# Optimization experiments

Hardware: AMD Instinct MI355X
Metric: run time of the kernel (lower is better)

## Reference

```python
import jax, jax.numpy as jnp
import numpy as np

B, L, F, H = 1024, 256, 128, 256
A, CH, OUT = 128, 256, 512


def setup_inputs() -> dict:
    key = jax.random.key(0)
    ks = jax.random.split(key, 12)
    s = lambda k, shape, fan: (jax.random.normal(k, shape, jnp.float32) / np.float32(np.sqrt(fan)))
    return dict(
        input_batch=jax.random.normal(ks[0], (B, L, F), jnp.float32),
        tte=jax.random.randint(ks[1], (B,), 0, L, jnp.int32),
        W_ih=s(ks[2], (3 * H, F), F), W_hh=s(ks[3], (3 * H, H), H),
        b_ih=jnp.zeros((3 * H,), jnp.float32), b_hh=jnp.zeros((3 * H,), jnp.float32),
        W_out=s(ks[4], (F, H), H), b_out=jnp.zeros((F,), jnp.float32),
        Wa=s(ks[5], (H, A), H), Ua=s(ks[6], (F, A), F), va=s(ks[7], (A,), A),
        W1=s(ks[8], (H + F, CH), H + F), b1=jnp.zeros((CH,), jnp.float32),
        W2=s(ks[9], (CH, OUT), CH), b2=jnp.zeros((OUT,), jnp.float32),
    )


def _gru_step(x, h, W_ih, W_hh, b_ih, b_hh):
    # torch.nn.GRU single-step math, batched over B
    gi = x @ W_ih.T + b_ih          # [B,3H]
    gh = h @ W_hh.T + b_hh          # [B,3H]
    i_r, i_z, i_n = jnp.split(gi, 3, axis=-1)
    h_r, h_z, h_n = jnp.split(gh, 3, axis=-1)
    r = jax.nn.sigmoid(i_r + h_r)
    z = jax.nn.sigmoid(i_z + h_z)
    n = jnp.tanh(i_n + r * h_n)
    return (1.0 - z) * n + z * h


def reference(input_batch, tte, W_ih, W_hh, b_ih, b_hh, W_out, b_out,
              Wa, Ua, va, W1, b1, W2, b2):
    Bn, Ln, Fn = input_batch.shape
    Hn = W_hh.shape[1]
    h0 = jnp.zeros((Bn, Hn), input_batch.dtype)
    xs = jnp.moveaxis(input_batch, 1, 0)  # [L,B,F]
    ts = jnp.arange(Ln)

    def step(h, inp):
        x_t, t = inp
        h_new = _gru_step(x_t, h, W_ih, W_hh, b_ih, b_hh)
        active = (t < tte)[:, None]          # ragged length mask [B,1]
        h = jnp.where(active, h_new, h)      # freeze state past tte
        out_t = jnp.where(active, h_new @ W_out.T + b_out, 0.0)
        hid_t = jnp.where(active, h_new, 0.0)
        return h, (out_t, hid_t)

    _, (outs, hids) = jax.lax.scan(step, h0, (xs, ts))
    output_batch = jnp.moveaxis(outs, 0, 1)   # [B,L,F], zero-padded like the torch code
    hidden_vec = jnp.moveaxis(hids, 0, 1)     # [B,L,H], zero-padded

    # last measurement at index tte (the torch code indexes batch[tte])
    last = jnp.take_along_axis(input_batch, tte[:, None, None].astype(jnp.int32), axis=1)[:, 0]  # [B,F]

    # decoder: additive attention over the full padded trajectory
    scores = jnp.tanh(hidden_vec @ Wa + (last @ Ua)[:, None, :]) @ va   # [B,L]
    alpha = jax.nn.softmax(scores, axis=-1)
    context = jnp.einsum('bl,blh->bh', alpha, hidden_vec)               # [B,H]

    # causes network: MLP + softmax over cause x time-bin grid
    zc = jax.nn.relu(jnp.concatenate([context, last], axis=-1) @ W1 + b1)
    fht = jax.nn.softmax(zc @ W2 + b2, axis=-1)                         # [B,OUT]
    return output_batch, fht
```

## Files before the change

kernel.cpp:

```cpp
#include <hip/hip_runtime.h>

#define B_ 1024
#define L_ 256
#define F_ 128
#define H_ 256

typedef __bf16 bf16x8 __attribute__((ext_vector_type(8)));
typedef __bf16 bf16x4 __attribute__((ext_vector_type(4)));
typedef float f32x4 __attribute__((ext_vector_type(4)));
typedef int i32x4 __attribute__((ext_vector_type(4)));

#define MFMA16(a, b, c) __builtin_amdgcn_mfma_f32_16x16x32_bf16((a), (b), (c), 0, 0, 0)
#define MFMA_I8(a, b, c) __builtin_amdgcn_mfma_i32_16x16x64_i8((a), (b), (c), 0, 0, 0)
#define BAR_LDS() asm volatile("s_waitcnt lgkmcnt(0)\n\ts_barrier" ::: "memory")

__device__ __forceinline__ float rcp_f(float x) { return __builtin_amdgcn_rcpf(x); }
__device__ __forceinline__ float sigm(float x) { return rcp_f(1.f + __expf(-x)); }
__device__ __forceinline__ float tanh_f(float x) {
  float ax = fabsf(x);
  float e = __expf(-2.f * ax);
  float r = (1.f - e) * rcp_f(1.f + e);
  return copysignf(r, x);
}
__device__ __forceinline__ bf16x8 ld8(const __bf16* p) { return *(const bf16x8*)p; }
__device__ __forceinline__ float wave_max(float v) {
#pragma unroll
  for (int d = 1; d < 64; d <<= 1) v = fmaxf(v, __shfl_xor(v, d));
  return v;
}
__device__ __forceinline__ float wave_sum(float v) {
#pragma unroll
  for (int d = 1; d < 64; d <<= 1) v += __shfl_xor(v, d);
  return v;
}
__device__ __forceinline__ unsigned pack4(float a, float b, float c, float d, float inv) {
  return (unsigned)(unsigned char)(signed char)__float2int_rn(a * inv)
       | ((unsigned)(unsigned char)(signed char)__float2int_rn(b * inv) << 8)
       | ((unsigned)(unsigned char)(signed char)__float2int_rn(c * inv) << 16)
       | ((unsigned)(unsigned char)(signed char)__float2int_rn(d * inv) << 24);
}
__device__ __forceinline__ void wait_flag(int* flags, int idx) {
  int guard = 0;
  while (__hip_atomic_load(&flags[idx], __ATOMIC_ACQUIRE, __HIP_MEMORY_SCOPE_AGENT) == 0)
    if (++guard > 2000000) break;
}

__global__ void cvt_kernel(const float* __restrict__ wih_f, const float* __restrict__ wout_f,
                           const float* __restrict__ wa_f, const float* __restrict__ ua_f,
                           const float* __restrict__ w1_f, const float* __restrict__ w2_f,
                           __bf16* __restrict__ wih, __bf16* __restrict__ wout,
                           __bf16* __restrict__ wa_t, __bf16* __restrict__ ua_t,
                           __bf16* __restrict__ w1_t, __bf16* __restrict__ w2_t) {
  int i = blockIdx.x * 256 + threadIdx.x;
  if (i < 98304) wih[i] = (__bf16)wih_f[i];
  else if (i < 131072) wout[i - 98304] = (__bf16)wout_f[i - 98304];
  else if (i < 163840) {
    int j = i - 131072; int a = j >> 8, k = j & 255;
    wa_t[j] = (__bf16)wa_f[k * 128 + a];
  } else if (i < 180224) {
    int j = i - 163840; int a = j >> 7, f = j & 127;
    ua_t[j] = (__bf16)ua_f[f * 128 + a];
  } else if (i < 278528) {
    int j = i - 180224; int c = j / 384, k = j - c * 384;
    w1_t[j] = (__bf16)w1_f[k * 256 + c];
  } else if (i < 409600) {
    int j = i - 278528; int o = j >> 8, k = j & 255;
    w2_t[j] = (__bf16)w2_f[k * 512 + o];
  }
}

__global__ void quant_kernel(const float* __restrict__ whh_f,
                             signed char* __restrict__ wq_rz,
                             signed char* __restrict__ wqn_f,
                             float* __restrict__ dq) {
  const int c = blockIdx.x * 256 + threadIdx.x;
  if (c >= 768) return;
  const float* row = whh_f + (size_t)c * 256;
  float m = 0.f;
  for (int k4 = 0; k4 < 64; ++k4) {
    float4 v = *(const float4*)(row + k4 * 4);
    m = fmaxf(m, fmaxf(fmaxf(fabsf(v.x), fabsf(v.y)), fmaxf(fabsf(v.z), fabsf(v.w))));
  }
  const float inv = (m > 1e-30f) ? 127.f / m : 0.f;
  dq[c] = m / 16129.f;
  if (c < 512) {
    for (int k4 = 0; k4 < 64; ++k4) {
      float4 v = *(const float4*)(row + k4 * 4);
      *(unsigned*)(wq_rz + (size_t)c * 256 + k4 * 4) = pack4(v.x, v.y, v.z, v.w, inv);
    }
  } else {
    const int cN = c - 512;
    const int base0 = (cN >> 4) * 4, l15q = cN & 15;
    for (int kt = 0; kt < 4; ++kt)
      for (int lgq = 0; lgq < 4; ++lgq) {
        signed char* dst = wqn_f + (size_t)(((base0 + kt) * 64) + lgq * 16 + l15q) * 16;
        const float* src = row + kt * 64 + lgq * 16;
        for (int j4 = 0; j4 < 4; ++j4) {
          float4 v = *(const float4*)(src + j4 * 4);
          *(unsigned*)(dst + j4 * 4) = pack4(v.x, v.y, v.z, v.w, inv);
        }
      }
  }
}

__global__ __launch_bounds__(1024) void mega_kernel(
    const float* __restrict__ x, const int* __restrict__ tte,
    const float* __restrict__ b_ih, const float* __restrict__ b_hh,
    const __bf16* __restrict__ wih,
    const signed char* __restrict__ wq_rz, const signed char* __restrict__ wqn_f,
    const float* __restrict__ dq, __bf16* __restrict__ gi,
    const __bf16* __restrict__ wout, const float* __restrict__ b_out,
    __bf16* __restrict__ hid, float* __restrict__ out, int* __restrict__ flags) {
  __shared__ signed char wlds[512 * 256];
  __shared__ signed char hb[2][16][272];
  __shared__ __bf16 hbf[2][16][260];
  const int tid = threadIdx.x;

  if (blockIdx.x >= 64) {
    const int pid = blockIdx.x - 64;
    const int bblk = pid & 63, tgrp = pid >> 6;
    const int b0 = bblk * 16;
    int tmaxB = 0;
    for (int i = 0; i < 16; ++i) tmaxB = max(tmaxB, tte[b0 + i]);
    if (tid < 512 && tgrp * 16 <= tmaxB) {
      const int lane = tid & 63, w = tid >> 6;
      const int l15 = lane & 15, lg = lane >> 4, kofs = lg * 8;
      bf16x8 wf[6][4];
      float bias[6];
#pragma unroll
      for (int tile = 0; tile < 6; ++tile) {
        const int gate = tile >> 1;
        const int c = w * 32 + (tile & 1) * 16 + l15;
        const int col = gate * 256 + c;
#pragma unroll
        for (int kt = 0; kt < 4; ++kt)
          wf[tile][kt] = ld8(wih + (size_t)col * 128 + kt * 32 + kofs);
        bias[tile] = (gate == 0) ? b_ih[c] + b_hh[c]
                   : (gate == 1) ? b_ih[256 + c] + b_hh[256 + c]
                                 : b_ih[512 + c];
      }
#pragma unroll 1
      for (int ti = 0; ti < 16; ++ti) {
        const int t = tgrp * 16 + ti;
        if (t > tmaxB) break;
        const float* xb = x + ((size_t)(b0 + l15) * L_ + t) * F_ + kofs;
        bf16x8 xfr[4];
#pragma unroll
        for (int kt = 0; kt < 4; ++kt) {
          float4 a = *(const float4*)(xb + kt * 32);
          float4 b = *(const float4*)(xb + kt * 32 + 4);
          xfr[kt][0] = (__bf16)a.x; xfr[kt][1] = (__bf16)a.y;
          xfr[kt][2] = (__bf16)a.z; xfr[kt][3] = (__bf16)a.w;
          xfr[kt][4] = (__bf16)b.x; xfr[kt][5] = (__bf16)b.y;
          xfr[kt][6] = (__bf16)b.z; xfr[kt][7] = (__bf16)b.w;
        }
        f32x4 acc[6];
#pragma unroll
        for (int tile = 0; tile < 6; ++tile) {
          acc[tile][0] = bias[tile]; acc[tile][1] = bias[tile];
          acc[tile][2] = bias[tile]; acc[tile][3] = bias[tile];
        }
#pragma unroll
        for (int kt = 0; kt < 4; ++kt)
#pragma unroll
          for (int tile = 0; tile < 6; ++tile)
            acc[tile] = MFMA16(xfr[kt], wf[tile][kt], acc[tile]);
        const size_t chunk = (((size_t)t * 64 + bblk) * 8 + w) * 6;
#pragma unroll
        for (int tile = 0; tile < 6; ++tile) {
          bf16x4 pk;
          pk[0] = (__bf16)acc[tile][0]; pk[1] = (__bf16)acc[tile][1];
          pk[2] = (__bf16)acc[tile][2]; pk[3] = (__bf16)acc[tile][3];
          *(bf16x4*)(gi + (chunk + tile) * 256 + (lg * 16 + l15) * 4) = pk;
        }
      }
    }
    __syncthreads();
    if (tid == 0)
      __hip_atomic_store(&flags[pid], 1, __ATOMIC_RELEASE, __HIP_MEMORY_SCOPE_AGENT);
    return;
  }

  const int lane = tid & 63, w = tid >> 6;
  const int l15 = lane & 15, lg = lane >> 4, kofs = lg * 8;
  const int b0 = blockIdx.x * 16;

  for (int idx = tid; idx < 8192; idx += 1024) {
    const int row = idx >> 4, g = idx & 15;
    uint4 v = *(const uint4*)(wq_rz + (size_t)row * 256 + g * 16);
    *(uint4*)&wlds[row * 256 + ((g ^ (row & 15)) << 4)] = v;
  }
  for (int i = tid; i < 2 * 16 * 272; i += 1024) ((signed char*)hb)[i] = 0;

  const int colL = w * 16 + l15;
  const float dqR = dq[colL], dqZ = dq[256 + colL], dqN = dq[512 + colL];
  const float bhn = b_hh[512 + colL];

  int tteC[4];
#pragma unroll
  for (int r = 0; r < 4; ++r) tteC[r] = tte[b0 + 4 * lg + r];
  const int rowS = (tid >> 5) & 15, segS = tid & 31;
  const int tteS = tte[b0 + rowS];
  int tmax = 0;
  for (int i = 0; i < 16; ++i) tmax = max(tmax, tte[b0 + i]);

  i32x4 nw[4];
#pragma unroll
  for (int kt = 0; kt < 4; ++kt)
    nw[kt] = *(const i32x4*)(wqn_f + (size_t)((w * 4 + kt) * 64 + lane) * 16);

  const int ocol = (w & 7) * 16 + l15;
  bf16x8 wof[8];
#pragma unroll
  for (int kt = 0; kt < 8; ++kt)
    wof[kt] = ld8(wout + (size_t)ocol * 256 + kt * 32 + kofs);
  const float bo = b_out[ocol];

  __bf16* hidp = hid + ((size_t)(b0 + rowS) * L_) * H_ + segS * 8;
  float* outp = out + ((size_t)(b0 + 4 * lg) * L_) * F_ + ocol;

  float hprev[4] = {0.f, 0.f, 0.f, 0.f};

  if (tid == 0) wait_flag(flags, blockIdx.x);
  __syncthreads();

  const __bf16* gib = gi + (((size_t)blockIdx.x * 8 + (w >> 1)) * 6 + (w & 1)) * 256
                    + (lg * 16 + l15) * 4;
  bf16x4 g0 = *(const bf16x4*)(gib);
  bf16x4 g1 = *(const bf16x4*)(gib + 512);
  bf16x4 g2 = *(const bf16x4*)(gib + 1024);
  const __bf16* gpp = gib + 786432;

#pragma unroll 1
  for (int t = 0; t < tmax; ++t) {
    const int c = t & 1, nc = c ^ 1;

    if (((t + 1) & 15) == 0) {
      if (tid == 0) wait_flag(flags, (((t + 1) >> 4) << 6) | blockIdx.x);
      __syncthreads();
    }

    const bf16x4 gr = g0, gz = g1, gn = g2;
    g0 = *(const bf16x4*)(gpp);
    g1 = *(const bf16x4*)(gpp + 512);
    g2 = *(const bf16x4*)(gpp + 1024);
    gpp += 786432;

    i32x4 aR = {0, 0, 0, 0}, aZ = {0, 0, 0, 0}, aN = {0, 0, 0, 0};
#pragma unroll
    for (int kt = 0; kt < 4; ++kt) {
      const i32x4 hA = *(const i32x4*)&hb[c][l15][kt * 64 + lg * 16];
      const int gsw = ((kt * 4 + lg) ^ l15) << 4;
      aR = MFMA_I8(hA, *(const i32x4*)&wlds[colL * 256 + gsw], aR);
      aZ = MFMA_I8(hA, *(const i32x4*)&wlds[(256 + colL) * 256 + gsw], aZ);
      aN = MFMA_I8(hA, nw[kt], aN);
    }

#pragma unroll
    for (int r = 0; r < 4; ++r) {
      const int row = 4 * lg + r;
      const float rg = sigm((float)gr[r] + (float)aR[r] * dqR);
      const float zg = sigm((float)gz[r] + (float)aZ[r] * dqZ);
      const float ng = tanh_f((float)gn[r] + rg * ((float)aN[r] * dqN + bhn));
      const float hold = hprev[r];
      const float hnew = zg * (hold - ng) + ng;
      const float hw = (t < tteC[r]) ? hnew : hold;
      hprev[r] = hw;
      hb[nc][row][colL] = (signed char)__float2int_rn(hw * 127.f);
      hbf[nc][row][colL] = (__bf16)hw;
    }
    BAR_LDS();

    if (w < 8) {
      f32x4 acc = {0, 0, 0, 0};
#pragma unroll
      for (int kt = 0; kt < 8; ++kt) {
        const bf16x8 af = *(const bf16x8*)&hbf[nc][l15][kt * 32 + kofs];
        acc = MFMA16(af, wof[kt], acc);
      }
#pragma unroll
      for (int r = 0; r < 4; ++r)
        if (t < tteC[r]) outp[(size_t)r * (L_ * F_)] = acc[r] + bo;
      outp += F_;
    } else {
      if (t < tteS) *(uint4*)hidp = *(const uint4*)&hbf[nc][rowS][segS * 8];
      hidp += H_;
    }
  }
}

__global__ __launch_bounds__(512, 2) void decoder3_kernel(
    const float* __restrict__ x, const int* __restrict__ tte,
    const __bf16* __restrict__ hid, const __bf16* __restrict__ wa_t,
    const __bf16* __restrict__ ua_t, const __bf16* __restrict__ w1_t,
    const __bf16* __restrict__ w2_t, const float* __restrict__ va,
    const float* __restrict__ b1, const float* __restrict__ b2,
    float* __restrict__ fht) {
  __shared__ __bf16 catb[16][392];
  __shared__ float u_s[4][128];
  __shared__ float sa[4][256];
  __shared__ __bf16 z1b[16][264];
  __shared__ float lg2[4][516];
  __shared__ float ctxp[2][4][256];
  __shared__ float va_s[128];
  __shared__ int tte_s[4];
  const int tid = threadIdx.x;
  const int lane = tid & 63, w = tid >> 6;
  const int l15 = lane & 15, lg = lane >> 4, kofs = lg * 8;
  const int b0 = blockIdx.x * 4;

  if (tid < 4) tte_s[tid] = tte[b0 + tid];
  if (tid < 128) va_s[tid] = va[tid];
  if (tid < 392)
    for (int r = 4; r < 16; ++r) catb[r][tid] = (__bf16)0.f;
  if (tid < 264)
    for (int r = 4; r < 16; ++r) z1b[r][tid] = (__bf16)0.f;
  __syncthreads();

  {
    const int row = tid >> 7, c = tid & 127;
    catb[row][256 + c] = (__bf16)x[((size_t)(b0 + row) * L_ + tte_s[row]) * F_ + c];
  }
  __syncthreads();

  {
    f32x4 uacc = {0, 0, 0, 0};
#pragma unroll
    for (int kt = 0; kt < 4; ++kt) {
      const bf16x8 af = *(const bf16x8*)&catb[l15][256 + kt * 32 + kofs];
      const bf16x8 bf = ld8(ua_t + (size_t)(w * 16 + l15) * 128 + kt * 32 + kofs);
      uacc = MFMA16(af, bf, uacc);
    }
#pragma unroll
    for (int r = 0; r < 4; ++r) {
      const int row = 4 * lg + r;
      if (row < 4) u_s[row][w * 16 + l15] = uacc[r];
    }
  }
  __syncthreads();

  bf16x8 zero8;
#pragma unroll
  for (int j = 0; j < 8; ++j) zero8[j] = (__bf16)0.f;
#pragma unroll 1
  for (int it = 0; it < 8; ++it) {
    const int pair = it * 8 + w;
    const int b = pair >> 4, mtile = pair & 15;
    const int tteB = tte_s[b];
    const int trow = mtile * 16 + l15;
    const __bf16* hrow = hid + ((size_t)(b0 + b) * L_ + trow) * H_ + kofs;
    bf16x8 af[8];
#pragma unroll
    for (int kt = 0; kt < 8; ++kt) af[kt] = (trow < tteB) ? ld8(hrow + kt * 32) : zero8;
    f32x4 sacc[8];
#pragma unroll
    for (int ct = 0; ct < 8; ++ct) { sacc[ct][0] = 0; sacc[ct][1] = 0; sacc[ct][2] = 0; sacc[ct][3] = 0; }
#pragma unroll
    for (int kt = 0; kt < 8; ++kt)
#pragma unroll
      for (int ct = 0; ct < 8; ++ct)
        sacc[ct] = MFMA16(af[kt], ld8(wa_t + (size_t)(ct * 16 + l15) * 256 + kt * 32 + kofs), sacc[ct]);
    float sp[4] = {0, 0, 0, 0};
#pragma unroll
    for (int ct = 0; ct < 8; ++ct) {
      const int a = ct * 16 + l15;
      const float ua = u_s[b][a], vv = va_s[a];
#pragma unroll
      for (int r = 0; r < 4; ++r) sp[r] += tanh_f(sacc[ct][r] + ua) * vv;
    }
#pragma unroll
    for (int r = 0; r < 4; ++r) {
      sp[r] += __shfl_xor(sp[r], 1);
      sp[r] += __shfl_xor(sp[r], 2);
      sp[r] += __shfl_xor(sp[r], 4);
      sp[r] += __shfl_xor(sp[r], 8);
    }
    if (l15 == 0) {
#pragma unroll
      for (int r = 0; r < 4; ++r) sa[b][mtile * 16 + 4 * lg + r] = sp[r];
    }
  }
  __syncthreads();

  if (w < 4) {
    float sv[4];
#pragma unroll
    for (int j = 0; j < 4; ++j) sv[j] = sa[w][lane + 64 * j];
    float mx = fmaxf(fmaxf(sv[0], sv[1]), fmaxf(sv[2], sv[3]));
    mx = wave_max(mx);
    float es[4], ss = 0.f;
#pragma unroll
    for (int j = 0; j < 4; ++j) { es[j] = __expf(sv[j] - mx); ss += es[j]; }
    ss = wave_sum(ss);
    const float inv = rcp_f(ss);
#pragma unroll
    for (int j = 0; j < 4; ++j) sa[w][lane + 64 * j] = es[j] * inv;
  }
  __syncthreads();

  {
    const int be = w & 3, half = w >> 2;
    const int tteE = tte_s[be];
    float c4[4] = {0.f, 0.f, 0.f, 0.f};
    const __bf16* hp = hid + ((size_t)(b0 + be) * L_ + half) * H_ + lane * 4;
#pragma unroll 2
    for (int t = half; t < tteE; t += 2) {
      const float al = sa[be][t];
      const bf16x4 hv = *(const bf16x4*)hp;
      hp += 2 * H_;
#pragma unroll
      for (int j = 0; j < 4; ++j) c4[j] += al * (float)hv[j];
    }
#pragma unroll
    for (int j = 0; j < 4; ++j) ctxp[half][be][lane * 4 + j] = c4[j];
  }
  __syncthreads();
  if (w < 4) {
#pragma unroll
    for (int j = 0; j < 4; ++j)
      catb[w][lane * 4 + j] = (__bf16)(ctxp[0][w][lane * 4 + j] + ctxp[1][w][lane * 4 + j]);
  }
  __syncthreads();

#pragma unroll 1
  for (int half = 0; half < 2; ++half) {
    const int nt = w * 2 + half;
    f32x4 zacc = {0, 0, 0, 0};
#pragma unroll
    for (int kt = 0; kt < 12; ++kt) {
      const bf16x8 af = *(const bf16x8*)&catb[l15][kt * 32 + kofs];
      const bf16x8 bf = ld8(w1_t + (size_t)(nt * 16 + l15) * 384 + kt * 32 + kofs);
      zacc = MFMA16(af, bf, zacc);
    }
    const float bb = b1[nt * 16 + l15];
#pragma unroll
    for (int r = 0; r < 4; ++r) {
      const int row = 4 * lg + r;
      if (row < 4) z1b[row][nt * 16 + l15] = (__bf16)fmaxf(zacc[r] + bb, 0.f);
    }
  }
  __syncthreads();

#pragma unroll 1
  for (int q = 0; q < 4; ++q) {
    const int nt = w * 4 + q;
    f32x4 oacc = {0, 0, 0, 0};
#pragma unroll
    for (int kt = 0; kt < 8; ++kt) {
      const bf16x8 af = *(const bf16x8*)&z1b[l15][kt * 32 + kofs];
      const bf16x8 bf = ld8(w2_t + (size_t)(nt * 16 + l15) * 256 + kt * 32 + kofs);
      oacc = MFMA16(af, bf, oacc);
    }
    const float bb = b2[nt * 16 + l15];
#pragma unroll
    for (int r = 0; r < 4; ++r) {
      const int row = 4 * lg + r;
      if (row < 4) lg2[row][nt * 16 + l15] = oacc[r] + bb;
    }
  }
  __syncthreads();
  if (w < 4) {
    float lv[8];
    float mx = -1e30f;
#pragma unroll
    for (int j = 0; j < 8; ++j) { lv[j] = lg2[w][lane + 64 * j]; mx = fmaxf(mx, lv[j]); }
    mx = wave_max(mx);
    float s2 = 0.f;
#pragma unroll
    for (int j = 0; j < 8; ++j) { lv[j] = __expf(lv[j] - mx); s2 += lv[j]; }
    s2 = wave_sum(s2);
    const float inv2 = rcp_f(s2);
#pragma unroll
    for (int j = 0; j < 8; ++j)
      fht[(size_t)(b0 + w) * 512 + lane + 64 * j] = lv[j] * inv2;
  }
}

extern "C" void kernel_launch(void* const* d_in, const int* in_sizes, int n_in,
                              void* d_out, int out_size, void* d_ws, size_t ws_size,
                              hipStream_t stream) {
  const float* x = (const float*)d_in[0];
  const int* tte = (const int*)d_in[1];
  const float* W_ih = (const float*)d_in[2];
  const float* W_hh = (const float*)d_in[3];
  const float* b_ih = (const float*)d_in[4];
  const float* b_hh = (const float*)d_in[5];
  const float* W_out = (const float*)d_in[6];
  const float* b_out = (const float*)d_in[7];
  const float* Wa = (const float*)d_in[8];
  const float* Ua = (const float*)d_in[9];
  const float* va = (const float*)d_in[10];
  const float* W1 = (const float*)d_in[11];
  const float* b1 = (const float*)d_in[12];
  const float* W2 = (const float*)d_in[13];
  const float* b2 = (const float*)d_in[14];

  char* ws = (char*)d_ws;
  __bf16* wih = (__bf16*)(ws + 0);
  __bf16* wout = (__bf16*)(ws + 196608);
  __bf16* wa_t = (__bf16*)(ws + 262144);
  __bf16* ua_t = (__bf16*)(ws + 327680);
  __bf16* w1_t = (__bf16*)(ws + 360448);
  __bf16* w2_t = (__bf16*)(ws + 557056);
  signed char* wq_rz = (signed char*)(ws + 819200);
  signed char* wqn_f = (signed char*)(ws + 950272);
  float* dq = (float*)(ws + 1015808);
  int* flags = (int*)(ws + 1018880);
  __bf16* hid = (__bf16*)(ws + 1048576);
  __bf16* gi = (__bf16*)(ws + 135266304);

  float* out = (float*)d_out;
  float* fht = out + (size_t)33554432;

  hipMemsetAsync(d_out, 0, (size_t)out_size * 4, stream);
  hipMemsetAsync(flags, 0, 4096, stream);
  cvt_kernel<<<1600, 256, 0, stream>>>(W_ih, W_out, Wa, Ua, W1, W2,
                                       wih, wout, wa_t, ua_t, w1_t, w2_t);
  quant_kernel<<<3, 256, 0, stream>>>(W_hh, wq_rz, wqn_f, dq);
  mega_kernel<<<1088, 1024, 0, stream>>>(x, tte, b_ih, b_hh, wih, wq_rz, wqn_f,
                                         dq, gi, wout, b_out, hid, out, flags);
  decoder3_kernel<<<256, 512, 0, stream>>>(x, tte, hid, wa_t, ua_t, w1_t, w2_t,
                                           va, b1, b2, fht);
}
```

Baseline: 876.8 us.

## Split GRU into separate gi GEMM and 4-row recurrent kernel over 256 blocks

Replaces the flag-synchronised megakernel with a standalone input-gate GEMM kernel followed by a recurrent kernel. Each recurrent block now handles 4 batch rows instead of 16, which spreads the sequential recurrence over 256 blocks instead of 64. Gate math is redistributed to one element per thread via an LDS staging buffer, at the cost of an extra barrier per step. The output projection is quantised to int8 MFMA, and the full output memset is replaced by zeroing only the padded rows inside the GEMM kernel. The int8 output projection adds quantisation error, and the GEMM can no longer overlap with the recurrence.

```diff
diff --git a/kernel.cpp b/kernel.cpp
--- a/kernel.cpp
+++ b/kernel.cpp
@@ -39,43 +39,38 @@
        | ((unsigned)(unsigned char)(signed char)__float2int_rn(c * inv) << 16)
        | ((unsigned)(unsigned char)(signed char)__float2int_rn(d * inv) << 24);
 }
-__device__ __forceinline__ void wait_flag(int* flags, int idx) {
-  int guard = 0;
-  while (__hip_atomic_load(&flags[idx], __ATOMIC_ACQUIRE, __HIP_MEMORY_SCOPE_AGENT) == 0)
-    if (++guard > 2000000) break;
-}
-
-__global__ void cvt_kernel(const float* __restrict__ wih_f, const float* __restrict__ wout_f,
-                           const float* __restrict__ wa_f, const float* __restrict__ ua_f,
-                           const float* __restrict__ w1_f, const float* __restrict__ w2_f,
-                           __bf16* __restrict__ wih, __bf16* __restrict__ wout,
-                           __bf16* __restrict__ wa_t, __bf16* __restrict__ ua_t,
-                           __bf16* __restrict__ w1_t, __bf16* __restrict__ w2_t) {
+
+__global__ void cvt_kernel(const float* __restrict__ wih_f, const float* __restrict__ wa_f,
+                           const float* __restrict__ ua_f, const float* __restrict__ w1_f,
+                           const float* __restrict__ w2_f,
+                           __bf16* __restrict__ wih, __bf16* __restrict__ wa_t,
+                           __bf16* __restrict__ ua_t, __bf16* __restrict__ w1_t,
+                           __bf16* __restrict__ w2_t) {
   int i = blockIdx.x * 256 + threadIdx.x;
   if (i < 98304) wih[i] = (__bf16)wih_f[i];
-  else if (i < 131072) wout[i - 98304] = (__bf16)wout_f[i - 98304];
-  else if (i < 163840) {
-    int j = i - 131072; int a = j >> 8, k = j & 255;
+  else if (i < 131072) {
+    int j = i - 98304; int a = j >> 8, k = j & 255;
     wa_t[j] = (__bf16)wa_f[k * 128 + a];
-  } else if (i < 180224) {
-    int j = i - 163840; int a = j >> 7, f = j & 127;
+  } else if (i < 147456) {
+    int j = i - 131072; int a = j >> 7, f = j & 127;
     ua_t[j] = (__bf16)ua_f[f * 128 + a];
-  } else if (i < 278528) {
-    int j = i - 180224; int c = j / 384, k = j - c * 384;
+  } else if (i < 245760) {
+    int j = i - 147456; int c = j / 384, k = j - c * 384;
     w1_t[j] = (__bf16)w1_f[k * 256 + c];
-  } else if (i < 409600) {
-    int j = i - 278528; int o = j >> 8, k = j & 255;
+  } else if (i < 376832) {
+    int j = i - 245760; int o = j >> 8, k = j & 255;
     w2_t[j] = (__bf16)w2_f[k * 512 + o];
   }
 }
 
-__global__ void quant_kernel(const float* __restrict__ whh_f,
+__global__ void quant_kernel(const float* __restrict__ whh_f, const float* __restrict__ wout_f,
                              signed char* __restrict__ wq_rz,
                              signed char* __restrict__ wqn_f,
+                             signed char* __restrict__ wqo_f,
                              float* __restrict__ dq) {
   const int c = blockIdx.x * 256 + threadIdx.x;
-  if (c >= 768) return;
-  const float* row = whh_f + (size_t)c * 256;
+  if (c >= 896) return;
+  const float* row = (c < 768) ? whh_f + (size_t)c * 256 : wout_f + (size_t)(c - 768) * 256;
   float m = 0.f;
   for (int k4 = 0; k4 < 64; ++k4) {
     float4 v = *(const float4*)(row + k4 * 4);
@@ -88,204 +83,223 @@
       float4 v = *(const float4*)(row + k4 * 4);
       *(unsigned*)(wq_rz + (size_t)c * 256 + k4 * 4) = pack4(v.x, v.y, v.z, v.w, inv);
     }
-  } else {
+  } else if (c < 768) {
     const int cN = c - 512;
-    const int base0 = (cN >> 4) * 4, l15q = cN & 15;
+    const int t16 = cN >> 4, l15q = cN & 15;
     for (int kt = 0; kt < 4; ++kt)
       for (int lgq = 0; lgq < 4; ++lgq) {
-        signed char* dst = wqn_f + (size_t)(((base0 + kt) * 64) + lgq * 16 + l15q) * 16;
+        signed char* dst = wqn_f + (size_t)(((t16 * 4 + kt) * 64) + lgq * 16 + l15q) * 16;
         const float* src = row + kt * 64 + lgq * 16;
         for (int j4 = 0; j4 < 4; ++j4) {
           float4 v = *(const float4*)(src + j4 * 4);
           *(unsigned*)(dst + j4 * 4) = pack4(v.x, v.y, v.z, v.w, inv);
         }
       }
-  }
-}
-
-__global__ __launch_bounds__(1024) void mega_kernel(
-    const float* __restrict__ x, const int* __restrict__ tte,
-    const float* __restrict__ b_ih, const float* __restrict__ b_hh,
-    const __bf16* __restrict__ wih,
-    const signed char* __restrict__ wq_rz, const signed char* __restrict__ wqn_f,
-    const float* __restrict__ dq, __bf16* __restrict__ gi,
-    const __bf16* __restrict__ wout, const float* __restrict__ b_out,
-    __bf16* __restrict__ hid, float* __restrict__ out, int* __restrict__ flags) {
-  __shared__ signed char wlds[512 * 256];
-  __shared__ signed char hb[2][16][272];
-  __shared__ __bf16 hbf[2][16][260];
-  const int tid = threadIdx.x;
-
-  if (blockIdx.x >= 64) {
-    const int pid = blockIdx.x - 64;
-    const int bblk = pid & 63, tgrp = pid >> 6;
-    const int b0 = bblk * 16;
-    int tmaxB = 0;
-    for (int i = 0; i < 16; ++i) tmaxB = max(tmaxB, tte[b0 + i]);
-    if (tid < 512 && tgrp * 16 <= tmaxB) {
-      const int lane = tid & 63, w = tid >> 6;
-      const int l15 = lane & 15, lg = lane >> 4, kofs = lg * 8;
-      bf16x8 wf[6][4];
-      float bias[6];
-#pragma unroll
-      for (int tile = 0; tile < 6; ++tile) {
-        const int gate = tile >> 1;
-        const int c = w * 32 + (tile & 1) * 16 + l15;
-        const int col = gate * 256 + c;
-#pragma unroll
-        for (int kt = 0; kt < 4; ++kt)
-          wf[tile][kt] = ld8(wih + (size_t)col * 128 + kt * 32 + kofs);
-        bias[tile] = (gate == 0) ? b_ih[c] + b_hh[c]
-                   : (gate == 1) ? b_ih[256 + c] + b_hh[256 + c]
-                                 : b_ih[512 + c];
-      }
-#pragma unroll 1
-      for (int ti = 0; ti < 16; ++ti) {
-        const int t = tgrp * 16 + ti;
-        if (t > tmaxB) break;
-        const float* xb = x + ((size_t)(b0 + l15) * L_ + t) * F_ + kofs;
-        bf16x8 xfr[4];
-#pragma unroll
-        for (int kt = 0; kt < 4; ++kt) {
-          float4 a = *(const float4*)(xb + kt * 32);
-          float4 b = *(const float4*)(xb + kt * 32 + 4);
-          xfr[kt][0] = (__bf16)a.x; xfr[kt][1] = (__bf16)a.y;
-          xfr[kt][2] = (__bf16)a.z; xfr[kt][3] = (__bf16)a.w;
-          xfr[kt][4] = (__bf16)b.x; xfr[kt][5] = (__bf16)b.y;
-          xfr[kt][6] = (__bf16)b.z; xfr[kt][7] = (__bf16)b.w;
-        }
-        f32x4 acc[6];
-#pragma unroll
-        for (int tile = 0; tile < 6; ++tile) {
-          acc[tile][0] = bias[tile]; acc[tile][1] = bias[tile];
-          acc[tile][2] = bias[tile]; acc[tile][3] = bias[tile];
-        }
-#pragma unroll
-        for (int kt = 0; kt < 4; ++kt)
-#pragma unroll
-          for (int tile = 0; tile < 6; ++tile)
-            acc[tile] = MFMA16(xfr[kt], wf[tile][kt], acc[tile]);
-        const size_t chunk = (((size_t)t * 64 + bblk) * 8 + w) * 6;
-#pragma unroll
-        for (int tile = 0; tile < 6; ++tile) {
-          bf16x4 pk;
-          pk[0] = (__bf16)acc[tile][0]; pk[1] = (__bf16)acc[tile][1];
-          pk[2] = (__bf16)acc[tile][2]; pk[3] = (__bf16)acc[tile][3];
-          *(bf16x4*)(gi + (chunk + tile) * 256 + (lg * 16 + l15) * 4) = pk;
+  } else {
+    const int oc = c - 768;
+    const int t8 = oc >> 4, l15q = oc & 15;
+    for (int kt = 0; kt < 4; ++kt)
+      for (int lgq = 0; lgq < 4; ++lgq) {
+        signed char* dst = wqo_f + (size_t)(((t8 * 4 + kt) * 64) + lgq * 16 + l15q) * 16;
+        const float* src = row + kt * 64 + lgq * 16;
+        for (int j4 = 0; j4 < 4; ++j4) {
+          float4 v = *(const float4*)(src + j4 * 4);
+          *(unsigned*)(dst + j4 * 4) = pack4(v.x, v.y, v.z, v.w, inv);
         }
       }
-    }
-    __syncthreads();
-    if (tid == 0)
-      __hip_atomic_store(&flags[pid], 1, __ATOMIC_RELEASE, __HIP_MEMORY_SCOPE_AGENT);
-    return;
-  }
-
+  }
+}
+
+__global__ __launch_bounds__(512, 2) void gi_gemm_kernel(
+    const float* __restrict__ x, const float* __restrict__ b_ih,
+    const float* __restrict__ b_hh, const __bf16* __restrict__ wih,
+    const int* __restrict__ tte, __bf16* __restrict__ gi,
+    float* __restrict__ out) {
+  const int tid = threadIdx.x;
   const int lane = tid & 63, w = tid >> 6;
   const int l15 = lane & 15, lg = lane >> 4, kofs = lg * 8;
-  const int b0 = blockIdx.x * 16;
+  const int bblk = blockIdx.x & 63, tgrp = blockIdx.x >> 6;
+  const int b0 = bblk * 16;
+
+  {
+    const int pr = tid >> 1, ph = tid & 1;
+    const int bl = pr >> 4, tl = pr & 15;
+    const int bb = b0 + bl, tt = tgrp * 16 + tl;
+    if (tt >= tte[bb]) {
+      float4* dst = (float4*)(out + ((size_t)bb * L_ + tt) * F_) + ph * 16;
+#pragma unroll
+      for (int i = 0; i < 16; ++i) dst[i] = float4{0.f, 0.f, 0.f, 0.f};
+    }
+  }
+
+  int tmaxB = 0;
+  for (int i = 0; i < 16; ++i) tmaxB = max(tmaxB, tte[b0 + i]);
+  if (tgrp * 16 > tmaxB) return;
+
+  bf16x8 wf[6][4];
+  float bias[6];
+#pragma unroll
+  for (int tile = 0; tile < 6; ++tile) {
+    const int gate = tile >> 1;
+    const int c = w * 32 + (tile & 1) * 16 + l15;
+    const int col = gate * 256 + c;
+#pragma unroll
+    for (int kt = 0; kt < 4; ++kt) wf[tile][kt] = ld8(wih + (size_t)col * 128 + kt * 32 + kofs);
+    bias[tile] = (gate == 0) ? b_ih[c] + b_hh[c]
+               : (gate == 1) ? b_ih[256 + c] + b_hh[256 + c]
+                             : b_ih[512 + c];
+  }
+
+#pragma unroll 1
+  for (int ti = 0; ti < 16; ++ti) {
+    const int t = tgrp * 16 + ti;
+    if (t > tmaxB) break;
+    const float* xb = x + ((size_t)(b0 + l15) * L_ + t) * F_ + kofs;
+    bf16x8 xfr[4];
+#pragma unroll
+    for (int kt = 0; kt < 4; ++kt) {
+      float4 a = *(const float4*)(xb + kt * 32);
+      float4 b = *(const float4*)(xb + kt * 32 + 4);
+      xfr[kt][0] = (__bf16)a.x; xfr[kt][1] = (__bf16)a.y;
+      xfr[kt][2] = (__bf16)a.z; xfr[kt][3] = (__bf16)a.w;
+      xfr[kt][4] = (__bf16)b.x; xfr[kt][5] = (__bf16)b.y;
+      xfr[kt][6] = (__bf16)b.z; xfr[kt][7] = (__bf16)b.w;
+    }
+    f32x4 acc[6];
+#pragma unroll
+    for (int tile = 0; tile < 6; ++tile) {
+      acc[tile][0] = bias[tile]; acc[tile][1] = bias[tile];
+      acc[tile][2] = bias[tile]; acc[tile][3] = bias[tile];
+    }
+#pragma unroll
+    for (int kt = 0; kt < 4; ++kt)
+#pragma unroll
+      for (int tile = 0; tile < 6; ++tile)
+        acc[tile] = MFMA16(xfr[kt], wf[tile][kt], acc[tile]);
+
+    const size_t chunk = (((size_t)t * 64 + bblk) * 8 + w) * 6;
+#pragma unroll
+    for (int tile = 0; tile < 6; ++tile) {
+      bf16x4 pk;
+      pk[0] = (__bf16)acc[tile][0]; pk[1] = (__bf16)acc[tile][1];
+      pk[2] = (__bf16)acc[tile][2]; pk[3] = (__bf16)acc[tile][3];
+      *(bf16x4*)(gi + (chunk + tile) * 256 + (lg * 16 + l15) * 4) = pk;
+    }
+  }
+}
+
+__global__ __launch_bounds__(1024) void gru256_kernel(
+    const int* __restrict__ tte, const float* __restrict__ b_hh,
+    const signed char* __restrict__ wq_rz, const signed char* __restrict__ wqn_f,
+    const signed char* __restrict__ wqo_f, const float* __restrict__ dq,
+    const __bf16* __restrict__ gi, const float* __restrict__ b_out,
+    __bf16* __restrict__ hid, float* __restrict__ out) {
+  __shared__ signed char wlds[512 * 256];
+  __shared__ signed char hb[2][4][272];
+  __shared__ f32x4 racc[4][256];
+  const int tid = threadIdx.x;
+  const int lane = tid & 63, w = tid >> 6;
+  const int l15 = lane & 15, lg = lane >> 4;
+  const int blk = blockIdx.x;
+  const int b0 = blk * 4;
 
   for (int idx = tid; idx < 8192; idx += 1024) {
     const int row = idx >> 4, g = idx & 15;
     uint4 v = *(const uint4*)(wq_rz + (size_t)row * 256 + g * 16);
     *(uint4*)&wlds[row * 256 + ((g ^ (row & 15)) << 4)] = v;
   }
-  for (int i = tid; i < 2 * 16 * 272; i += 1024) ((signed char*)hb)[i] = 0;
+  for (int i = tid; i < 2 * 4 * 272; i += 1024) ((signed char*)hb)[i] = 0;
 
   const int colL = w * 16 + l15;
-  const float dqR = dq[colL], dqZ = dq[256 + colL], dqN = dq[512 + colL];
-  const float bhn = b_hh[512 + colL];
-
-  int tteC[4];
-#pragma unroll
-  for (int r = 0; r < 4; ++r) tteC[r] = tte[b0 + 4 * lg + r];
-  const int rowS = (tid >> 5) & 15, segS = tid & 31;
-  const int tteS = tte[b0 + rowS];
-  int tmax = 0;
-  for (int i = 0; i < 16; ++i) tmax = max(tmax, tte[b0 + i]);
-
   i32x4 nw[4];
 #pragma unroll
   for (int kt = 0; kt < 4; ++kt)
     nw[kt] = *(const i32x4*)(wqn_f + (size_t)((w * 4 + kt) * 64 + lane) * 16);
 
   const int ocol = (w & 7) * 16 + l15;
-  bf16x8 wof[8];
-#pragma unroll
-  for (int kt = 0; kt < 8; ++kt)
-    wof[kt] = ld8(wout + (size_t)ocol * 256 + kt * 32 + kofs);
+  i32x4 ow[4];
+#pragma unroll
+  for (int kt = 0; kt < 4; ++kt)
+    ow[kt] = *(const i32x4*)(wqo_f + (size_t)(((w & 7) * 4 + kt) * 64 + lane) * 16);
+  const float dqo = dq[768 + ocol];
   const float bo = b_out[ocol];
-
-  __bf16* hidp = hid + ((size_t)(b0 + rowS) * L_) * H_ + segS * 8;
-  float* outp = out + ((size_t)(b0 + 4 * lg) * L_) * F_ + ocol;
-
-  float hprev[4] = {0.f, 0.f, 0.f, 0.f};
-
-  if (tid == 0) wait_flag(flags, blockIdx.x);
-  __syncthreads();
-
-  const __bf16* gib = gi + (((size_t)blockIdx.x * 8 + (w >> 1)) * 6 + (w & 1)) * 256
-                    + (lg * 16 + l15) * 4;
-  bf16x4 g0 = *(const bf16x4*)(gib);
-  bf16x4 g1 = *(const bf16x4*)(gib + 512);
-  bf16x4 g2 = *(const bf16x4*)(gib + 1024);
-  const __bf16* gpp = gib + 786432;
+  int tteO[4];
+#pragma unroll
+  for (int r = 0; r < 4; ++r) tteO[r] = tte[b0 + r];
+  float* outp = out + ((size_t)b0 * L_) * F_ + ocol;
+
+  const int grow = tid >> 8, gcol = tid & 255;
+  const float dqR = dq[gcol], dqZ = dq[256 + gcol], dqN = dq[512 + gcol];
+  const float bhn = b_hh[512 + gcol];
+  const int tteL = tte[b0 + grow];
+  int tmax = 0;
+#pragma unroll
+  for (int i = 0; i < 4; ++i) tmax = max(tmax, tte[b0 + i]);
+
+  const size_t gb0 = (((size_t)(blk >> 2) * 8 + (gcol >> 5)) * 6 + ((gcol >> 4) & 1)) * 256
+                   + (size_t)((blk & 3) * 16 + (gcol & 15)) * 4 + grow;
+  const __bf16* gp = gi + gb0;
+  __bf16 gR = gp[0], gZ = gp[512], gN = gp[1024];
+  const __bf16* gpp = gp + 786432;
+
+  __bf16* hidp = hid + ((size_t)(b0 + grow) * L_) * H_ + gcol;
+  float hprev = 0.f;
+
+  __syncthreads();
 
 #pragma unroll 1
   for (int t = 0; t < tmax; ++t) {
     const int c = t & 1, nc = c ^ 1;
 
-    if (((t + 1) & 15) == 0) {
-      if (tid == 0) wait_flag(flags, (((t + 1) >> 4) << 6) | blockIdx.x);
-      __syncthreads();
-    }
-
-    const bf16x4 gr = g0, gz = g1, gn = g2;
-    g0 = *(const bf16x4*)(gpp);
-    g1 = *(const bf16x4*)(gpp + 512);
-    g2 = *(const bf16x4*)(gpp + 1024);
-    gpp += 786432;
-
     i32x4 aR = {0, 0, 0, 0}, aZ = {0, 0, 0, 0}, aN = {0, 0, 0, 0};
 #pragma unroll
     for (int kt = 0; kt < 4; ++kt) {
-      const i32x4 hA = *(const i32x4*)&hb[c][l15][kt * 64 + lg * 16];
+      const i32x4 hA = *(const i32x4*)&hb[c][l15 & 3][kt * 64 + lg * 16];
       const int gsw = ((kt * 4 + lg) ^ l15) << 4;
       aR = MFMA_I8(hA, *(const i32x4*)&wlds[colL * 256 + gsw], aR);
       aZ = MFMA_I8(hA, *(const i32x4*)&wlds[(256 + colL) * 256 + gsw], aZ);
       aN = MFMA_I8(hA, nw[kt], aN);
     }
-
-#pragma unroll
-    for (int r = 0; r < 4; ++r) {
-      const int row = 4 * lg + r;
-      const float rg = sigm((float)gr[r] + (float)aR[r] * dqR);
-      const float zg = sigm((float)gz[r] + (float)aZ[r] * dqZ);
-      const float ng = tanh_f((float)gn[r] + rg * ((float)aN[r] * dqN + bhn));
-      const float hold = hprev[r];
-      const float hnew = zg * (hold - ng) + ng;
-      const float hw = (t < tteC[r]) ? hnew : hold;
-      hprev[r] = hw;
-      hb[nc][row][colL] = (signed char)__float2int_rn(hw * 127.f);
-      hbf[nc][row][colL] = (__bf16)hw;
+    if (lg == 0) {
+#pragma unroll
+      for (int r = 0; r < 4; ++r) {
+        f32x4 v = {(float)aR[r], (float)aZ[r], (float)aN[r], 0.f};
+        racc[r][colL] = v;
+      }
     }
     BAR_LDS();
 
+    {
+      const f32x4 rv = racc[grow][gcol];
+      const float grf = (float)gR, gzf = (float)gZ, gnf = (float)gN;
+      gR = gpp[0]; gZ = gpp[512]; gN = gpp[1024];
+      gpp += 786432;
+      const float rg = sigm(grf + rv[0] * dqR);
+      const float zg = sigm(gzf + rv[1] * dqZ);
+      const float ng = tanh_f(gnf + rg * (rv[2] * dqN + bhn));
+      const float hnew = zg * (hprev - ng) + ng;
+      const float hw = (t < tteL) ? hnew : hprev;
+      hprev = hw;
+      hb[nc][grow][gcol] = (signed char)__float2int_rn(hw * 127.f);
+      if (t < tteL) *hidp = (__bf16)hw;
+      hidp += H_;
+    }
+    BAR_LDS();
+
     if (w < 8) {
-      f32x4 acc = {0, 0, 0, 0};
-#pragma unroll
-      for (int kt = 0; kt < 8; ++kt) {
-        const bf16x8 af = *(const bf16x8*)&hbf[nc][l15][kt * 32 + kofs];
-        acc = MFMA16(af, wof[kt], acc);
+      i32x4 ac = {0, 0, 0, 0};
+#pragma unroll
+      for (int kt = 0; kt < 4; ++kt) {
+        const i32x4 hA = *(const i32x4*)&hb[nc][l15 & 3][kt * 64 + lg * 16];
+        ac = MFMA_I8(hA, ow[kt], ac);
       }
-#pragma unroll
-      for (int r = 0; r < 4; ++r)
-        if (t < tteC[r]) outp[(size_t)r * (L_ * F_)] = acc[r] + bo;
-      outp += F_;
-    } else {
-      if (t < tteS) *(uint4*)hidp = *(const uint4*)&hbf[nc][rowS][segS * 8];
-      hidp += H_;
-    }
+      if (lg == 0) {
+#pragma unroll
+        for (int r = 0; r < 4; ++r)
+          if (t < tteO[r]) outp[(size_t)r * (L_ * F_)] = (float)ac[r] * dqo + bo;
+      }
+    }
+    outp += F_;
   }
 }
 
@@ -497,28 +511,26 @@
 
   char* ws = (char*)d_ws;
   __bf16* wih = (__bf16*)(ws + 0);
-  __bf16* wout = (__bf16*)(ws + 196608);
-  __bf16* wa_t = (__bf16*)(ws + 262144);
-  __bf16* ua_t = (__bf16*)(ws + 327680);
-  __bf16* w1_t = (__bf16*)(ws + 360448);
-  __bf16* w2_t = (__bf16*)(ws + 557056);
-  signed char* wq_rz = (signed char*)(ws + 819200);
-  signed char* wqn_f = (signed char*)(ws + 950272);
-  float* dq = (float*)(ws + 1015808);
-  int* flags = (int*)(ws + 1018880);
+  __bf16* wa_t = (__bf16*)(ws + 196608);
+  __bf16* ua_t = (__bf16*)(ws + 262144);
+  __bf16* w1_t = (__bf16*)(ws + 294912);
+  __bf16* w2_t = (__bf16*)(ws + 491520);
+  signed char* wq_rz = (signed char*)(ws + 753664);
+  signed char* wqn_f = (signed char*)(ws + 884736);
+  signed char* wqo_f = (signed char*)(ws + 950272);
+  float* dq = (float*)(ws + 983040);
   __bf16* hid = (__bf16*)(ws + 1048576);
   __bf16* gi = (__bf16*)(ws + 135266304);
 
   float* out = (float*)d_out;
   float* fht = out + (size_t)33554432;
 
-  hipMemsetAsync(d_out, 0, (size_t)out_size * 4, stream);
-  hipMemsetAsync(flags, 0, 4096, stream);
-  cvt_kernel<<<1600, 256, 0, stream>>>(W_ih, W_out, Wa, Ua, W1, W2,
-                                       wih, wout, wa_t, ua_t, w1_t, w2_t);
-  quant_kernel<<<3, 256, 0, stream>>>(W_hh, wq_rz, wqn_f, dq);
-  mega_kernel<<<1088, 1024, 0, stream>>>(x, tte, b_ih, b_hh, wih, wq_rz, wqn_f,
-                                         dq, gi, wout, b_out, hid, out, flags);
+  cvt_kernel<<<1472, 256, 0, stream>>>(W_ih, Wa, Ua, W1, W2,
+                                       wih, wa_t, ua_t, w1_t, w2_t);
+  quant_kernel<<<4, 256, 0, stream>>>(W_hh, W_out, wq_rz, wqn_f, wqo_f, dq);
+  gi_gemm_kernel<<<1024, 512, 0, stream>>>(x, b_ih, b_hh, wih, tte, gi, out);
+  gru256_kernel<<<256, 1024, 0, stream>>>(tte, b_hh, wq_rz, wqn_f, wqo_f, dq,
+                                          gi, b_out, hid, out);
   decoder3_kernel<<<256, 512, 0, stream>>>(x, tte, hid, wa_t, ua_t, w1_t, w2_t,
                                            va, b1, b2, fht);
 }
```

Result: faster. 793.5 us (-9.5%).
